# Performance work log

Hardware: AMD Instinct MI355X
Metric: run time of the kernel (lower is better)

Reference implementation:

```python
import jax, jax.numpy as jnp
import numpy as np

EMBEDS = 195  # C, also used in the (unusual) 1/sqrt(C) scale


def setup_inputs() -> dict:
    key = jax.random.key(0)
    k1, k2, k3, k4 = jax.random.split(key, 4)
    B, T, C, H = 1024, 256, EMBEDS, 8
    x = jax.random.normal(k1, (B, T, C), dtype=jnp.float32)
    Wq = jax.random.normal(k2, (C, H), dtype=jnp.float32) * 0.05
    Wk = jax.random.normal(k3, (C, H), dtype=jnp.float32) * 0.05
    Wv = jax.random.normal(k4, (C, H), dtype=jnp.float32) * 0.05
    return {"x": x, "Wq": Wq, "Wk": Wk, "Wv": Wv}


def reference(x, Wq, Wk, Wv):
    B, T, C = x.shape
    q = jnp.einsum('btc,ch->bth', x, Wq)  # [B,T,H]
    k = jnp.einsum('btc,ch->bth', x, Wk)
    v = jnp.einsum('btc,ch->bth', x, Wv)
    # scores scaled by 1/sqrt(C) (embedding dim), faithful to source
    scores = jnp.einsum('bqh,bkh->bqk', q, k) * (1.0 / jnp.sqrt(jnp.float32(C)))
    causal = jnp.tril(jnp.ones((T, T), dtype=bool))  # [T,T]
    scores = jnp.where(causal, scores, -jnp.inf)
    attn = jax.nn.softmax(scores, axis=-1)
    # dropout treated as identity (eval mode) for deterministic reference
    out = jnp.einsum('bqk,bkh->bqh', attn, v)
    return out
```

## Files before the change

kernel.cpp:

```cpp
#include <hip/hip_runtime.h>
#include <hip/hip_bf16.h>
#include <stdint.h>

#define TT   256
#define CC   195
#define HH   8
#define NKT  7
#define VSTR 260

typedef __attribute__((ext_vector_type(8))) short short8;
typedef __attribute__((ext_vector_type(4))) short short4v;
typedef __attribute__((ext_vector_type(4))) float f32x4;

static __device__ __forceinline__ short f2bf(float v) {
    union { __hip_bfloat16 h; short s; } cv;
    cv.h = __float2bfloat16(v);
    return cv.s;
}

__global__ __launch_bounds__(256, 4)
void fused_head(const float* __restrict__ x,
                const float* __restrict__ Wq,
                const float* __restrict__ Wk,
                const float* __restrict__ Wv,
                float* __restrict__ out)
{
    __shared__ short Ql[TT * 8];
    __shared__ short Kl[TT * 8];
    __shared__ short Vt[16 * VSTR];

    const int tid  = threadIdx.x;
    const int lane = tid & 63;
    const int wv   = __builtin_amdgcn_readfirstlane(tid >> 6);
    const int b    = blockIdx.x;
    const int nn   = lane & 15;
    const int quad = lane >> 4;

    {
        uint32_t* vtw = (uint32_t*)Vt;
        const int base = (8 * VSTR) / 2;
        for (int i = tid; i < (8 * VSTR) / 2; i += 256)
            vtw[base + i] = (i < VSTR / 2) ? 0x3F803F80u : 0u;
    }

    const float* __restrict__ xb = x + (size_t)b * (TT * CC);

    const float* Wsel0 = (nn < 8) ? (Wq + nn) : (Wk + nn - 8);
    const float* Wsel1 = (nn < 8) ? (Wv + nn) : nullptr;
    short8 Bf[NKT][2];
#pragma unroll
    for (int kt = 0; kt < NKT; ++kt) {
#pragma unroll
        for (int j = 0; j < 8; ++j) {
            const int k = kt * 32 + quad * 8 + j;
            float v0 = (k < CC) ? Wsel0[(size_t)k * HH] : 0.f;
            float v1 = (k < CC && Wsel1) ? Wsel1[(size_t)k * HH] : 0.f;
            Bf[kt][0][j] = f2bf(v0);
            Bf[kt][1][j] = f2bf(v1);
        }
    }

    auto proj_ch = [&](int ch) {
        const int rbase = ch * 64 + wv * 16;
        const float* __restrict__ xrow = xb + (size_t)(rbase + nn) * CC;

        f32x4 acc0 = {0.f, 0.f, 0.f, 0.f};
        f32x4 acc1 = {0.f, 0.f, 0.f, 0.f};
#pragma unroll
        for (int kt = 0; kt < NKT; ++kt) {
            float f[8];
#pragma unroll
            for (int j = 0; j < 8; ++j) {
                const int k = kt * 32 + quad * 8 + j;
                f[j] = (k < CC) ? xrow[k] : 0.f;
            }
            short8 a;
#pragma unroll
            for (int j = 0; j < 8; ++j) a[j] = f2bf(f[j]);
            acc0 = __builtin_amdgcn_mfma_f32_16x16x32_bf16(a, Bf[kt][0], acc0, 0, 0, 0);
            acc1 = __builtin_amdgcn_mfma_f32_16x16x32_bf16(a, Bf[kt][1], acc1, 0, 0, 0);
        }
#pragma unroll
        for (int r = 0; r < 4; ++r) {
            const int trow = rbase + quad * 4 + r;
            const short qs = f2bf(acc0[r]);
            if (nn < 8) {
                Ql[trow * 8 + nn] = qs;
                Vt[nn * VSTR + trow] = f2bf(acc1[r]);
            } else {
                Kl[trow * 8 + (nn - 8)] = qs;
            }
        }
    };

    const float SC2 = 0.07161149f * 1.44269504f;

    auto attn_tile = [&](int qt) {
        const int qb = qt * 16;
        const int qcol = qb + nn;

        short8 bQ = (short8){0, 0, 0, 0, 0, 0, 0, 0};
        if (quad == 0)
            bQ = *reinterpret_cast<const short8*>(Ql + (qb + nn) * 8);

        f32x4 accO = {0.f, 0.f, 0.f, 0.f};
        const int nch = (qt >> 1) + 1;
        for (int c = 0; c < nch; ++c) {
            const int kb = c * 32;
            const bool doH1 = (c < nch - 1) || (qt & 1);

            short8 aK0 = (short8){0, 0, 0, 0, 0, 0, 0, 0};
            short8 aK1 = (short8){0, 0, 0, 0, 0, 0, 0, 0};
            if (quad == 0) {
                aK0 = *reinterpret_cast<const short8*>(Kl + (kb + nn) * 8);
                if (doH1)
                    aK1 = *reinterpret_cast<const short8*>(Kl + (kb + 16 + nn) * 8);
            }
            f32x4 s0 = __builtin_amdgcn_mfma_f32_16x16x32_bf16(
                           aK0, bQ, (f32x4){0.f, 0.f, 0.f, 0.f}, 0, 0, 0);
            f32x4 s1 = {0.f, 0.f, 0.f, 0.f};
            if (doH1)
                s1 = __builtin_amdgcn_mfma_f32_16x16x32_bf16(
                         aK1, bQ, (f32x4){0.f, 0.f, 0.f, 0.f}, 0, 0, 0);

            const short* vrow = Vt + nn * VSTR + kb + quad * 4;
            const short4v v0 = *reinterpret_cast<const short4v*>(vrow);
            const short4v v1 = *reinterpret_cast<const short4v*>(vrow + 16);

            const int keyb = kb + quad * 4;
            short8 aP, bV;
#pragma unroll
            for (int r = 0; r < 4; ++r) {
                const float e0 = (keyb + r <= qcol) ? exp2f(s0[r] * SC2) : 0.f;
                const float e1 = (doH1 && (keyb + 16 + r <= qcol))
                                     ? exp2f(s1[r] * SC2) : 0.f;
                aP[r]     = f2bf(e0);
                aP[4 + r] = f2bf(e1);
                bV[r]     = v0[r];
                bV[4 + r] = v1[r];
            }
            accO = __builtin_amdgcn_mfma_f32_16x16x32_bf16(aP, bV, accO, 0, 0, 0);
        }

#pragma unroll
        for (int r = 0; r < 4; ++r) {
            const float dn = __shfl(accO[r], (lane & 48) | 8);
            if (nn < 8) {
                const int q = qb + quad * 4 + r;
                out[((size_t)b * TT + q) * HH + nn] = accO[r] / dn;
            }
        }
    };

    proj_ch(0);
    __syncthreads();
    proj_ch(1);
    attn_tile(wv);
    __syncthreads();
    proj_ch(2);
    attn_tile(4 + (wv ^ 1));
    __syncthreads();
    proj_ch(3);
    attn_tile(8 + (wv ^ 2));
    __syncthreads();
    attn_tile(12 + (wv ^ 3));
}

extern "C" void kernel_launch(void* const* d_in, const int* in_sizes, int n_in,
                              void* d_out, int out_size, void* d_ws, size_t ws_size,
                              hipStream_t stream)
{
    const float* x  = (const float*)d_in[0];
    const float* Wq = (const float*)d_in[1];
    const float* Wk = (const float*)d_in[2];
    const float* Wv = (const float*)d_in[3];
    float* out      = (float*)d_out;
    const int B = in_sizes[0] / (TT * CC);
    fused_head<<<dim3(B), dim3(256), 0, stream>>>(x, Wq, Wk, Wv, out);
}
```

Measured before the change: 305.5 us.

## Prefetch next x chunk into registers and stage bf16 weights in LDS

Splits the projection into issue and consume phases, so the global loads of x for the next 64-row chunk are in flight while the current chunk's attention tile and MFMAs run. Weight fragments are converted to bf16 once per block, with each wave handling a subset, and stored in LDS. This replaces the per-thread register array of 14 short8 fragments, freeing registers for the prefetch buffer. The cost is extra LDS traffic for the weight reads, a larger register buffer for x, and hand-placed barriers and sched_barriers that constrain the compiler's scheduling.

```diff
diff --git a/kernel.cpp b/kernel.cpp
--- a/kernel.cpp
+++ b/kernel.cpp
@@ -2,11 +2,13 @@
 #include <hip/hip_bf16.h>
 #include <stdint.h>
 
-#define TT   256
-#define CC   195
-#define HH   8
-#define NKT  7
-#define VSTR 260
+#define TT    256
+#define CC    195
+#define HH    8
+#define NKT   7
+#define VSTR  260
+#define WSETS 14
+#define WLSTR 40
 
 typedef __attribute__((ext_vector_type(8))) short short8;
 typedef __attribute__((ext_vector_type(4))) short short4v;
@@ -25,9 +27,10 @@
                 const float* __restrict__ Wv,
                 float* __restrict__ out)
 {
-    __shared__ short Ql[TT * 8];
-    __shared__ short Kl[TT * 8];
-    __shared__ short Vt[16 * VSTR];
+    __shared__ __align__(16) short Ql[TT * 8];
+    __shared__ __align__(16) short Kl[TT * 8];
+    __shared__ __align__(16) short Vt[16 * VSTR];
+    __shared__ __align__(16) short Wl[WSETS * 16 * WLSTR];
 
     const int tid  = threadIdx.x;
     const int lane = tid & 63;
@@ -36,49 +39,36 @@
     const int nn   = lane & 15;
     const int quad = lane >> 4;
 
-    {
-        uint32_t* vtw = (uint32_t*)Vt;
-        const int base = (8 * VSTR) / 2;
-        for (int i = tid; i < (8 * VSTR) / 2; i += 256)
-            vtw[base + i] = (i < VSTR / 2) ? 0x3F803F80u : 0u;
-    }
-
     const float* __restrict__ xb = x + (size_t)b * (TT * CC);
 
-    const float* Wsel0 = (nn < 8) ? (Wq + nn) : (Wk + nn - 8);
-    const float* Wsel1 = (nn < 8) ? (Wv + nn) : nullptr;
-    short8 Bf[NKT][2];
-#pragma unroll
-    for (int kt = 0; kt < NKT; ++kt) {
-#pragma unroll
-        for (int j = 0; j < 8; ++j) {
-            const int k = kt * 32 + quad * 8 + j;
-            float v0 = (k < CC) ? Wsel0[(size_t)k * HH] : 0.f;
-            float v1 = (k < CC && Wsel1) ? Wsel1[(size_t)k * HH] : 0.f;
-            Bf[kt][0][j] = f2bf(v0);
-            Bf[kt][1][j] = f2bf(v1);
-        }
-    }
-
-    auto proj_ch = [&](int ch) {
+    float xp[NKT][8];
+
+    auto issue = [&](int ch) {
+        const float* __restrict__ xrow = xb + (size_t)(ch * 64 + wv * 16 + nn) * CC;
+#pragma unroll
+        for (int kt = 0; kt < NKT; ++kt)
+#pragma unroll
+            for (int j = 0; j < 8; ++j) {
+                const int k = kt * 32 + quad * 8 + j;
+                xp[kt][j] = (k < CC) ? xrow[k] : 0.f;
+            }
+    };
+
+    auto consume = [&](int ch) {
         const int rbase = ch * 64 + wv * 16;
-        const float* __restrict__ xrow = xb + (size_t)(rbase + nn) * CC;
-
         f32x4 acc0 = {0.f, 0.f, 0.f, 0.f};
         f32x4 acc1 = {0.f, 0.f, 0.f, 0.f};
 #pragma unroll
         for (int kt = 0; kt < NKT; ++kt) {
-            float f[8];
-#pragma unroll
-            for (int j = 0; j < 8; ++j) {
-                const int k = kt * 32 + quad * 8 + j;
-                f[j] = (k < CC) ? xrow[k] : 0.f;
-            }
             short8 a;
 #pragma unroll
-            for (int j = 0; j < 8; ++j) a[j] = f2bf(f[j]);
-            acc0 = __builtin_amdgcn_mfma_f32_16x16x32_bf16(a, Bf[kt][0], acc0, 0, 0, 0);
-            acc1 = __builtin_amdgcn_mfma_f32_16x16x32_bf16(a, Bf[kt][1], acc1, 0, 0, 0);
+            for (int j = 0; j < 8; ++j) a[j] = f2bf(xp[kt][j]);
+            const short8 b0 = *reinterpret_cast<const short8*>(
+                Wl + ((kt * 2 + 0) * 16 + nn) * WLSTR + quad * 8);
+            const short8 b1 = *reinterpret_cast<const short8*>(
+                Wl + ((kt * 2 + 1) * 16 + nn) * WLSTR + quad * 8);
+            acc0 = __builtin_amdgcn_mfma_f32_16x16x32_bf16(a, b0, acc0, 0, 0, 0);
+            acc1 = __builtin_amdgcn_mfma_f32_16x16x32_bf16(a, b1, acc1, 0, 0, 0);
         }
 #pragma unroll
         for (int r = 0; r < 4; ++r) {
@@ -152,17 +142,63 @@
         }
     };
 
-    proj_ch(0);
-    __syncthreads();
-    proj_ch(1);
+    auto barrier_lds = [&]() {
+        asm volatile("s_waitcnt lgkmcnt(0)" ::: "memory");
+        __builtin_amdgcn_s_barrier();
+        __builtin_amdgcn_sched_barrier(0);
+    };
+
+    issue(0);
+    __builtin_amdgcn_sched_barrier(0);
+
+    {
+        uint32_t* vtw = (uint32_t*)Vt;
+        const int base = (8 * VSTR) / 2;
+        for (int i = tid; i < (8 * VSTR) / 2; i += 256)
+            vtw[base + i] = (i < VSTR / 2) ? 0x3F803F80u : 0u;
+    }
+    {
+        const float* Wsel0 = (nn < 8) ? (Wq + nn) : (Wk + nn - 8);
+        const float* Wsel1 = Wv + (nn & 7);
+        for (int set = wv; set < WSETS; set += 4) {
+            const int kt = set >> 1, sv = set & 1;
+            short8 frag;
+#pragma unroll
+            for (int j = 0; j < 8; ++j) {
+                const int k = kt * 32 + quad * 8 + j;
+                float v = 0.f;
+                if (k < CC) {
+                    if (sv == 0)        v = Wsel0[(size_t)k * HH];
+                    else if (nn < 8)    v = Wsel1[(size_t)k * HH];
+                }
+                frag[j] = f2bf(v);
+            }
+            *reinterpret_cast<short8*>(Wl + (set * 16 + nn) * WLSTR + quad * 8) = frag;
+        }
+    }
+    barrier_lds();
+
+    consume(0);
+    issue(1);
+    __builtin_amdgcn_sched_barrier(0);
+    barrier_lds();
+
     attn_tile(wv);
-    __syncthreads();
-    proj_ch(2);
+    consume(1);
+    issue(2);
+    __builtin_amdgcn_sched_barrier(0);
+    barrier_lds();
+
     attn_tile(4 + (wv ^ 1));
-    __syncthreads();
-    proj_ch(3);
+    consume(2);
+    issue(3);
+    __builtin_amdgcn_sched_barrier(0);
+    barrier_lds();
+
     attn_tile(8 + (wv ^ 2));
-    __syncthreads();
+    consume(3);
+    barrier_lds();
+
     attn_tile(12 + (wv ^ 3));
 }
 
```

After: 297.5 us, median of 2. 2.6% less time.
